# Kernel tuning notes

Measured on AMD Instinct MI355X. Metric: run time of the kernel, lower is better.

Reference implementation:

```python
import jax, jax.numpy as jnp
import numpy as np

D_MODEL = 1024
NUM_HEADS = 16
ROPE_THETA = 10000.0


def setup_inputs() -> dict:
    key = jax.random.key(0)
    ks = jax.random.split(key, 5)
    B, S, D = 4, 2048, D_MODEL
    std = (2.0 / (D * D)) ** 0.5
    return {
        "x": jax.random.normal(ks[0], (B, S, D), dtype=jnp.float32),
        "Wq": jax.random.normal(ks[1], (D, D), dtype=jnp.float32) * std,
        "Wk": jax.random.normal(ks[2], (D, D), dtype=jnp.float32) * std,
        "Wv": jax.random.normal(ks[3], (D, D), dtype=jnp.float32) * std,
        "Wo": jax.random.normal(ks[4], (D, D), dtype=jnp.float32) * std,
    }


def _apply_rope(t, sin, cos):
    # t: [B, H, S, d_k]; sin/cos: [S, d_k//2] (broadcast over B, H)
    e = t[..., 0::2]
    o = t[..., 1::2]
    rot = jnp.stack((e * cos - o * sin, e * sin + o * cos), axis=-1)
    return rot.reshape(t.shape)  # interleave back to d_k


def reference(x, Wq, Wk, Wv, Wo):
    B, S, D = x.shape
    H = NUM_HEADS
    dk = D // H

    def proj(W):
        y = jnp.einsum('bsd,ed->bse', x, W)  # Linear: weight is [out, in]
        return y.reshape(B, S, H, dk).transpose(0, 2, 1, 3)  # [B,H,S,dk]

    q, k, v = proj(Wq), proj(Wk), proj(Wv)

    # RoPE cache (token_positions = arange(S))
    half = dk // 2
    inv_freq = 1.0 / (ROPE_THETA ** (jnp.arange(half, dtype=jnp.float32) * 2.0 / dk))
    angles = jnp.arange(S, dtype=jnp.float32)[:, None] * inv_freq[None, :]  # [S, half]
    sin, cos = jnp.sin(angles), jnp.cos(angles)
    q = _apply_rope(q, sin, cos)
    k = _apply_rope(k, sin, cos)

    # scaled dot-product attention with causal mask
    scores = jnp.einsum('bhqd,bhkd->bhqk', q, k) / jnp.sqrt(jnp.float32(dk))
    causal = jnp.tril(jnp.ones((S, S), dtype=bool))
    scores = jnp.where(causal, scores, jnp.finfo(scores.dtype).min)
    p = jax.nn.softmax(scores, axis=-1)
    out = jnp.einsum('bhqk,bhkd->bhqd', p, v)  # [B,H,S,dk]

    out = out.transpose(0, 2, 1, 3).reshape(B, S, D)
    return jnp.einsum('bsd,ed->bse', out, Wo)
```

## Files before the change

kernel.cpp:

```cpp
#include <hip/hip_runtime.h>

typedef unsigned short u16;
typedef unsigned int   u32;

typedef short    short8 __attribute__((ext_vector_type(8)));
typedef __bf16   bf16x8 __attribute__((ext_vector_type(8)));
typedef _Float16 half8  __attribute__((ext_vector_type(8)));
typedef float    f32x4  __attribute__((ext_vector_type(4)));

#define S_LEN   2048
#define DM      1024
#define NHEAD   16
#define DK      64
#define KDIM    1024

__device__ __forceinline__ u16 f2bf(float f) {
    u32 u = __builtin_bit_cast(u32, f);
    u += 0x7FFFu + ((u >> 16) & 1u);
    return (u16)(u >> 16);
}
__device__ __forceinline__ f32x4 mfma_bf16(short8 a, short8 b, f32x4 c) {
    return __builtin_amdgcn_mfma_f32_16x16x32_bf16(
        __builtin_bit_cast(bf16x8, a), __builtin_bit_cast(bf16x8, b), c, 0, 0, 0);
}
__device__ __forceinline__ f32x4 mfma_f16(half8 a, half8 b, f32x4 c) {
    return __builtin_amdgcn_mfma_f32_16x16x32_f16(a, b, c, 0, 0, 0);
}
__device__ __forceinline__ u32 pk_f16(float a, float b) {
    return __builtin_bit_cast(u32, __builtin_amdgcn_cvt_pkrtz(a, b));
}
__device__ __forceinline__ void gl_lds16(const void* g, void* l) {
    __builtin_amdgcn_global_load_lds(
        (const __attribute__((address_space(1))) u32*)g,
        (__attribute__((address_space(3))) u32*)l, 16, 0, 0);
}
__device__ __forceinline__ void bar_raw() { asm volatile("s_barrier" ::: "memory"); }
__device__ __forceinline__ void wait_vm4() { asm volatile("s_waitcnt vmcnt(4)" ::: "memory"); }
__device__ __forceinline__ void wait_vm0() { asm volatile("s_waitcnt vmcnt(0)" ::: "memory"); }

__device__ __forceinline__ int perm_inv(int rc) {
    const int nt = rc >> 4, mid = (rc >> 2) & 3, r = rc & 3;
    return 32 * (nt >> 1) + 8 * mid + 4 * (nt & 1) + r;
}

__global__ void cvt_all(const float4* __restrict__ x,  const float4* __restrict__ Wq,
                        const float4* __restrict__ Wk, const float4* __restrict__ Wv,
                        const float4* __restrict__ Wo,
                        uint2* __restrict__ oX, uint2* __restrict__ oWcat,
                        uint2* __restrict__ oWo,
                        float* __restrict__ sT, float* __restrict__ cT) {
    const int i = blockIdx.x * 256 + threadIdx.x;
    if (i < 3145728) {
        const float4* in;
        uint2* out;
        if (i < 2097152) {
            in = x + i;  out = oX + i;
        } else {
            const int j = i - 2097152;
            const int w = j >> 18, k = j & 262143;
            in  = (w == 0 ? Wq : w == 1 ? Wk : w == 2 ? Wv : Wo) + k;
            out = (w < 3) ? (oWcat + w * 262144 + k) : (oWo + k);
        }
        float4 f = *in;
        uint2 o;
        o.x = (u32)f2bf(f.x) | ((u32)f2bf(f.y) << 16);
        o.y = (u32)f2bf(f.z) | ((u32)f2bf(f.w) << 16);
        *out = o;
    } else {
        const int idx = i - 3145728;
        const float fi = expf(-(float)(idx >> 11) * 0.287823136624255f);
        const float ang = (float)(idx & 2047) * fi;
        sT[idx] = sinf(ang);
        cT[idx] = cosf(ang);
    }
}

template <int MODE>
__global__ __launch_bounds__(256)
void gemm_nt(const u16* __restrict__ A, const u16* __restrict__ Bw,
             u16* __restrict__ oQ, u16* __restrict__ oK, u16* __restrict__ oVt,
             float* __restrict__ oF,
             const float* __restrict__ ropeS, const float* __restrict__ ropeC) {
    __shared__ u16 As[2][128 * 32];
    __shared__ u16 Bs[2][128 * 32];
    const int tid  = threadIdx.x;
    const int wave = tid >> 6, lane = tid & 63;
    const int quad = lane >> 4, l15 = lane & 15;
    const int wr = wave >> 1, wc = wave & 1;
    const int NX  = (MODE == 0) ? 24 : 8;
    const int lin = (int)blockIdx.x + NX * (int)blockIdx.y;
    const int xcd = lin & 7, idx = lin >> 3;
    const int mbase = (xcd * 8 + idx / NX) * 128;
    const int nbase = (idx % NX) * 128;

    f32x4 acc[4][4];
#pragma unroll
    for (int i = 0; i < 4; i++)
#pragma unroll
        for (int j = 0; j < 4; j++) acc[i][j] = (f32x4)0.0f;

    const int srow0 = wave * 32 + (lane >> 2);
    const int srow1 = srow0 + 16;
    const int scolb = ((lane & 3) ^ ((lane >> 3) & 3)) * 16;
    const int ldsOff = wave * 2048 + lane * 16;
    const u16* gA0 = A  + (size_t)(mbase + srow0) * KDIM;
    const u16* gA1 = A  + (size_t)(mbase + srow1) * KDIM;
    const u16* gB0 = Bw + (size_t)(nbase + srow0) * KDIM;
    const u16* gB1 = Bw + (size_t)(nbase + srow1) * KDIM;
    const int koffq = (quad ^ ((l15 >> 1) & 3)) * 8;

    const int KT = KDIM / 64;
    for (int kt = 0; kt < KT; kt++) {
        const int kk = kt * 64;
        __syncthreads();
#pragma unroll
        for (int s = 0; s < 2; s++) {
            const int ko = kk + s * 32;
            gl_lds16((const char*)(gA0 + ko) + scolb, (char*)As[s] + ldsOff);
            gl_lds16((const char*)(gA1 + ko) + scolb, (char*)As[s] + ldsOff + 1024);
            gl_lds16((const char*)(gB0 + ko) + scolb, (char*)Bs[s] + ldsOff);
            gl_lds16((const char*)(gB1 + ko) + scolb, (char*)Bs[s] + ldsOff + 1024);
        }
        __syncthreads();

        short8 af[4][2], bf[4][2];
#pragma unroll
        for (int s = 0; s < 2; s++) {
#pragma unroll
            for (int mt = 0; mt < 4; mt++)
                af[mt][s] = *(const short8*)&As[s][(wr * 64 + mt * 16 + l15) * 32 + koffq];
#pragma unroll
            for (int nt = 0; nt < 4; nt++)
                bf[nt][s] = *(const short8*)&Bs[s][(wc * 64 + nt * 16 + l15) * 32 + koffq];
        }
#pragma unroll
        for (int s = 0; s < 2; s++)
#pragma unroll
            for (int mt = 0; mt < 4; mt++)
#pragma unroll
                for (int nt = 0; nt < 4; nt++)
                    acc[mt][nt] = mfma_bf16(af[mt][s], bf[nt][s], acc[mt][nt]);
    }

    const int proj_blk = (MODE == 0) ? (nbase >> 10) : 2;

    const float* sB[4];
    const float* cB[4];
    if (MODE == 0 && proj_blk < 2) {
#pragma unroll
        for (int nt = 0; nt < 4; nt++) {
            const int fi = nt * 8 + (l15 >> 1);
            sB[nt] = ropeS + fi * 2048;
            cB[nt] = ropeC + fi * 2048;
        }
    }
    const int par = l15 & 1;

#pragma unroll
    for (int mt = 0; mt < 4; mt++) {
#pragma unroll
        for (int nt = 0; nt < 4; nt++) {
            const int n  = nbase + wc * 64 + nt * 16 + l15;
            const int mb = mbase + wr * 64 + mt * 16 + quad * 4;
            f32x4 v = acc[mt][nt];
            if (MODE == 0) {
                const int e = n & 1023;
                const int h = e >> 6, d = e & 63;
                if (proj_blk == 2) {
                    const int b_ = mb >> 11, s = mb & 2047;
                    const int bh = b_ * NHEAD + h;
                    uint2 pk;
                    pk.x = pk_f16(v[0], v[1]);
                    pk.y = pk_f16(v[2], v[3]);
                    *(uint2*)&oVt[((size_t)bh * DK + d) * S_LEN + s] = pk;
                } else {
                    u16* dst = (proj_blk == 0) ? oQ : oK;
                    float vp[4];
#pragma unroll
                    for (int r = 0; r < 4; r++) vp[r] = __shfl_xor(v[r], 1);
                    const int b_ = mb >> 11, s0 = mb & 2047;
                    const int bh = b_ * NHEAD + h;
                    const f32x4 sn = *(const f32x4*)(sB[nt] + s0);
                    const f32x4 cs = *(const f32x4*)(cB[nt] + s0);
#pragma unroll
                    for (int r = 0; r < 4; r++) {
                        const float res = par ? (vp[r] * sn[r] + v[r] * cs[r])
                                              : (v[r] * cs[r] - vp[r] * sn[r]);
                        dst[((size_t)bh * S_LEN + (s0 + r)) * DK + d] = f2bf(res);
                    }
                }
            } else {
#pragma unroll
                for (int r = 0; r < 4; r++)
                    oF[(size_t)(mb + r) * DM + n] = v[r];
            }
        }
    }
}

__global__ __launch_bounds__(256)
void flash_attn(const u16* __restrict__ Q, const u16* __restrict__ K,
                const u16* __restrict__ Vt, u16* __restrict__ Oc) {
    __shared__ u16 Ks[2][64 * 64];
    __shared__ u16 Vs[2][64 * 64];
    const int lin = (int)blockIdx.x + 64 * (int)blockIdx.y;
    const int xcd = lin & 7, idx = lin >> 3;
    const int bh  = xcd * 8 + (idx & 7);
    const int qt  = 31 - (idx >> 3);
    const int tid  = threadIdx.x;
    const int wave = tid >> 6, lane = tid & 63;
    const int quad = lane >> 4, l15 = lane & 15;
    const int x7 = l15 & 7;
    const size_t headQK = (size_t)bh * S_LEN * DK;
    const size_t headVt = (size_t)bh * DK * S_LEN;
    const int b = bh >> 4, h = bh & 15;
    const float SCL = 0.18033688011112042f;
    const float THRESH = 44.3614195558365f;

    half8 ones;
#pragma unroll
    for (int j = 0; j < 8; j++) ones[j] = (_Float16)1.0f;

    const int rwl  = lane >> 3;
    const int scol = (lane & 7) ^ rwl;
    const int rc0 = wave * 16 + rwl, rc1 = rc0 + 8;
    const u16* gK0 = K  + headQK + (size_t)perm_inv(rc0) * DK + scol * 8;
    const u16* gK1 = K  + headQK + (size_t)perm_inv(rc1) * DK + scol * 8;
    const u16* gV0 = Vt + headVt + (size_t)rc0 * S_LEN + scol * 8;
    const u16* gV1 = Vt + headVt + (size_t)rc1 * S_LEN + scol * 8;
    const int ldsOff = wave * 2048 + lane * 16;
    const int koff0 = (quad ^ x7) * 8;
    const int koff1 = ((4 + quad) ^ x7) * 8;

    short8 qf0, qf1;
    {
        const int qrow = qt * 64 + wave * 16 + l15;
        qf0 = *(const short8*)&Q[headQK + (size_t)qrow * DK + quad * 8];
        qf1 = *(const short8*)&Q[headQK + (size_t)qrow * DK + 32 + quad * 8];
    }

    float m_st = -__builtin_inff();
    f32x4 lacc = (f32x4)0.0f;
    f32x4 oacc[4];
#pragma unroll
    for (int n = 0; n < 4; n++) oacc[n] = (f32x4)0.0f;

    const int NT = qt + 1;
    gl_lds16(gK0, (char*)Ks[0] + ldsOff);
    gl_lds16(gK1, (char*)Ks[0] + ldsOff + 1024);
    gl_lds16(gV0, (char*)Vs[0] + ldsOff);
    gl_lds16(gV1, (char*)Vs[0] + ldsOff + 1024);

    for (int kt = 0; kt < NT; kt++) {
        const int cur = kt & 1, nxt = cur ^ 1;
        bar_raw();
        {
            const int ktn = (kt + 1 < NT) ? kt + 1 : kt;
            gl_lds16(gK0 + (size_t)ktn * 64 * DK, (char*)Ks[nxt] + ldsOff);
            gl_lds16(gK1 + (size_t)ktn * 64 * DK, (char*)Ks[nxt] + ldsOff + 1024);
            gl_lds16(gV0 + ktn * 64,              (char*)Vs[nxt] + ldsOff);
            gl_lds16(gV1 + ktn * 64,              (char*)Vs[nxt] + ldsOff + 1024);
        }
        wait_vm4();
        bar_raw();

        f32x4 sc[4];
        __builtin_amdgcn_s_setprio(1);
#pragma unroll
        for (int nt = 0; nt < 4; nt++) {
            const int rb = (nt * 16 + l15) * 64;
            short8 kf0 = *(const short8*)&Ks[cur][rb + koff0];
            short8 kf1 = *(const short8*)&Ks[cur][rb + koff1];
            f32x4 z = (f32x4)0.0f;
            z = mfma_bf16(kf0, qf0, z);
            z = mfma_bf16(kf1, qf1, z);
            sc[nt] = z;
        }
        __builtin_amdgcn_s_setprio(0);

        if (kt == qt) {
            const int qloc = wave * 16 + l15;
#pragma unroll
            for (int nt = 0; nt < 4; nt++) {
                const int kb = 32 * (nt >> 1) + 8 * quad + 4 * (nt & 1);
#pragma unroll
                for (int r = 0; r < 4; r++)
                    if (kb + r > qloc) sc[nt][r] = -__builtin_inff();
            }
        }
        float mx0 = fmaxf(fmaxf(sc[0][0], sc[0][1]), fmaxf(sc[0][2], sc[0][3]));
        float mx1 = fmaxf(fmaxf(sc[1][0], sc[1][1]), fmaxf(sc[1][2], sc[1][3]));
        float mx2 = fmaxf(fmaxf(sc[2][0], sc[2][1]), fmaxf(sc[2][2], sc[2][3]));
        float mx3 = fmaxf(fmaxf(sc[3][0], sc[3][1]), fmaxf(sc[3][2], sc[3][3]));
        float mx = fmaxf(fmaxf(mx0, mx1), fmaxf(mx2, mx3));
        mx = fmaxf(mx, __shfl_xor(mx, 16));
        mx = fmaxf(mx, __shfl_xor(mx, 32));
        if (!__all(mx - m_st <= THRESH)) {
            const float mn = fmaxf(m_st, mx);
            const float alpha = __builtin_amdgcn_exp2f((m_st - mn) * SCL);
            m_st = mn;
            float alr[4];
#pragma unroll
            for (int r = 0; r < 4; r++) alr[r] = __shfl(alpha, quad * 20 + r);
#pragma unroll
            for (int n = 0; n < 4; n++)
#pragma unroll
                for (int r = 0; r < 4; r++) oacc[n][r] *= alr[r];
#pragma unroll
            for (int r = 0; r < 4; r++) lacc[r] *= alr[r];
        }
        const float msc = m_st * SCL;
#pragma unroll
        for (int nt = 0; nt < 4; nt++)
#pragma unroll
            for (int r = 0; r < 4; r++)
                sc[nt][r] = __builtin_amdgcn_exp2f(
                    __builtin_fmaf(sc[nt][r], SCL, -msc));
        u32 pw[8];
        pw[0] = pk_f16(sc[0][0], sc[0][1]); pw[1] = pk_f16(sc[0][2], sc[0][3]);
        pw[2] = pk_f16(sc[1][0], sc[1][1]); pw[3] = pk_f16(sc[1][2], sc[1][3]);
        pw[4] = pk_f16(sc[2][0], sc[2][1]); pw[5] = pk_f16(sc[2][2], sc[2][3]);
        pw[6] = pk_f16(sc[3][0], sc[3][1]); pw[7] = pk_f16(sc[3][2], sc[3][3]);
        half8 pf0 = __builtin_bit_cast(half8, *(uint4*)&pw[0]);
        half8 pf1 = __builtin_bit_cast(half8, *(uint4*)&pw[4]);

        __builtin_amdgcn_s_setprio(1);
#pragma unroll
        for (int c = 0; c < 2; c++) {
            const half8 pf = c ? pf1 : pf0;
            lacc = mfma_f16(pf, ones, lacc);
            const int voff = ((c * 4 + quad) ^ x7) * 8;
#pragma unroll
            for (int nt2 = 0; nt2 < 4; nt2++) {
                half8 vf = __builtin_bit_cast(half8,
                    *(const short8*)&Vs[cur][(nt2 * 16 + l15) * 64 + voff]);
                oacc[nt2] = mfma_f16(pf, vf, oacc[nt2]);
            }
        }
        __builtin_amdgcn_s_setprio(0);
    }
    wait_vm0();

#pragma unroll
    for (int r = 0; r < 4; r++) {
        const float inv = 1.0f / lacc[r];
        const int s = qt * 64 + wave * 16 + quad * 4 + r;
#pragma unroll
        for (int nt2 = 0; nt2 < 4; nt2++)
            Oc[((size_t)(b * S_LEN + s)) * DM + h * 64 + nt2 * 16 + l15] =
                f2bf(oacc[nt2][r] * inv);
    }
}

#define OFF_XBF   ((size_t)0)
#define OFF_WCAT  ((size_t)8388608)
#define OFF_WO    ((size_t)11534336)
#define OFF_QB    ((size_t)12582912)
#define OFF_KB    ((size_t)20971520)
#define OFF_VT    ((size_t)29360128)
#define OFF_ROPE  ((size_t)37748736)

extern "C" void kernel_launch(void* const* d_in, const int* in_sizes, int n_in,
                              void* d_out, int out_size, void* d_ws, size_t ws_size,
                              hipStream_t stream) {
    const float* x  = (const float*)d_in[0];
    const float* Wq = (const float*)d_in[1];
    const float* Wk = (const float*)d_in[2];
    const float* Wv = (const float*)d_in[3];
    const float* Wo = (const float*)d_in[4];
    u16* ws  = (u16*)d_ws;
    u16* XBF = ws + OFF_XBF;
    u16* WCA = ws + OFF_WCAT;
    u16* WOB = ws + OFF_WO;
    u16* QB  = ws + OFF_QB;
    u16* KB  = ws + OFF_KB;
    u16* VT  = ws + OFF_VT;
    float* ropeS = (float*)(ws + OFF_ROPE);
    float* ropeC = ropeS + 65536;
    u16* AT  = XBF;

    cvt_all<<<12544, 256, 0, stream>>>((const float4*)x, (const float4*)Wq,
                                       (const float4*)Wk, (const float4*)Wv,
                                       (const float4*)Wo,
                                       (uint2*)XBF, (uint2*)WCA, (uint2*)WOB,
                                       ropeS, ropeC);

    gemm_nt<0><<<dim3(24, 64), 256, 0, stream>>>(XBF, WCA, QB, KB, VT, nullptr,
                                                 ropeS, ropeC);
    flash_attn<<<dim3(64, 32), 256, 0, stream>>>(QB, KB, VT, AT);
    gemm_nt<1><<<dim3(8, 64), 256, 0, stream>>>(AT, WOB, nullptr, nullptr, nullptr,
                                                (float*)d_out, nullptr, nullptr);
}
```

Baseline: 257.0 us.

## Share K/V tiles across two query tiles with 512-thread attention blocks

Each flash-attention block now handles 128 query rows with 8 waves instead of 64 rows with 4 waves, so every K/V tile loaded into LDS serves twice as many queries. Each wave now issues half as many global-to-LDS loads per tile, and the wait count is adjusted to match. The lower half of the block skips the final K tile, which lies beyond its causal range. In exchange the grid halves, the causal load is split across blocks more coarsely, and lower-half waves idle at the barriers for that last tile.

```diff
diff --git a/kernel.cpp b/kernel.cpp
--- a/kernel.cpp
+++ b/kernel.cpp
@@ -35,7 +35,7 @@
         (__attribute__((address_space(3))) u32*)l, 16, 0, 0);
 }
 __device__ __forceinline__ void bar_raw() { asm volatile("s_barrier" ::: "memory"); }
-__device__ __forceinline__ void wait_vm4() { asm volatile("s_waitcnt vmcnt(4)" ::: "memory"); }
+__device__ __forceinline__ void wait_vm2() { asm volatile("s_waitcnt vmcnt(2)" ::: "memory"); }
 __device__ __forceinline__ void wait_vm0() { asm volatile("s_waitcnt vmcnt(0)" ::: "memory"); }
 
 __device__ __forceinline__ int perm_inv(int rc) {
@@ -198,7 +198,7 @@
     }
 }
 
-__global__ __launch_bounds__(256)
+__global__ __launch_bounds__(512)
 void flash_attn(const u16* __restrict__ Q, const u16* __restrict__ K,
                 const u16* __restrict__ Vt, u16* __restrict__ Oc) {
     __shared__ u16 Ks[2][64 * 64];
@@ -206,9 +206,10 @@
     const int lin = (int)blockIdx.x + 64 * (int)blockIdx.y;
     const int xcd = lin & 7, idx = lin >> 3;
     const int bh  = xcd * 8 + (idx & 7);
-    const int qt  = 31 - (idx >> 3);
+    const int qt  = 15 - (idx >> 3);
     const int tid  = threadIdx.x;
     const int wave = tid >> 6, lane = tid & 63;
+    const int hh   = wave >> 2, w4 = wave & 3;
     const int quad = lane >> 4, l15 = lane & 15;
     const int x7 = l15 & 7;
     const size_t headQK = (size_t)bh * S_LEN * DK;
@@ -223,18 +224,16 @@
 
     const int rwl  = lane >> 3;
     const int scol = (lane & 7) ^ rwl;
-    const int rc0 = wave * 16 + rwl, rc1 = rc0 + 8;
-    const u16* gK0 = K  + headQK + (size_t)perm_inv(rc0) * DK + scol * 8;
-    const u16* gK1 = K  + headQK + (size_t)perm_inv(rc1) * DK + scol * 8;
-    const u16* gV0 = Vt + headVt + (size_t)rc0 * S_LEN + scol * 8;
-    const u16* gV1 = Vt + headVt + (size_t)rc1 * S_LEN + scol * 8;
-    const int ldsOff = wave * 2048 + lane * 16;
+    const int rc   = wave * 8 + rwl;
+    const u16* gK = K  + headQK + (size_t)perm_inv(rc) * DK + scol * 8;
+    const u16* gV = Vt + headVt + (size_t)rc * S_LEN + scol * 8;
+    const int ldsOff = wave * 1024 + lane * 16;
     const int koff0 = (quad ^ x7) * 8;
     const int koff1 = ((4 + quad) ^ x7) * 8;
 
     short8 qf0, qf1;
     {
-        const int qrow = qt * 64 + wave * 16 + l15;
+        const int qrow = qt * 128 + hh * 64 + w4 * 16 + l15;
         qf0 = *(const short8*)&Q[headQK + (size_t)qrow * DK + quad * 8];
         qf1 = *(const short8*)&Q[headQK + (size_t)qrow * DK + 32 + quad * 8];
     }
@@ -245,24 +244,24 @@
 #pragma unroll
     for (int n = 0; n < 4; n++) oacc[n] = (f32x4)0.0f;
 
-    const int NT = qt + 1;
-    gl_lds16(gK0, (char*)Ks[0] + ldsOff);
-    gl_lds16(gK1, (char*)Ks[0] + ldsOff + 1024);
-    gl_lds16(gV0, (char*)Vs[0] + ldsOff);
-    gl_lds16(gV1, (char*)Vs[0] + ldsOff + 1024);
+    const int NT = 2 * qt + 2;
+    const int skip_kt = (hh == 0) ? (2 * qt + 1) : -1;
+    const int diag_kt = 2 * qt + hh;
+    gl_lds16(gK, (char*)Ks[0] + ldsOff);
+    gl_lds16(gV, (char*)Vs[0] + ldsOff);
 
     for (int kt = 0; kt < NT; kt++) {
         const int cur = kt & 1, nxt = cur ^ 1;
         bar_raw();
         {
             const int ktn = (kt + 1 < NT) ? kt + 1 : kt;
-            gl_lds16(gK0 + (size_t)ktn * 64 * DK, (char*)Ks[nxt] + ldsOff);
-            gl_lds16(gK1 + (size_t)ktn * 64 * DK, (char*)Ks[nxt] + ldsOff + 1024);
-            gl_lds16(gV0 + ktn * 64,              (char*)Vs[nxt] + ldsOff);
-            gl_lds16(gV1 + ktn * 64,              (char*)Vs[nxt] + ldsOff + 1024);
-        }
-        wait_vm4();
+            gl_lds16(gK + (size_t)ktn * 64 * DK, (char*)Ks[nxt] + ldsOff);
+            gl_lds16(gV + ktn * 64,              (char*)Vs[nxt] + ldsOff);
+        }
+        wait_vm2();
         bar_raw();
+
+        if (kt == skip_kt) continue;
 
         f32x4 sc[4];
         __builtin_amdgcn_s_setprio(1);
@@ -278,8 +277,8 @@
         }
         __builtin_amdgcn_s_setprio(0);
 
-        if (kt == qt) {
-            const int qloc = wave * 16 + l15;
+        if (kt == diag_kt) {
+            const int qloc = w4 * 16 + l15;
 #pragma unroll
             for (int nt = 0; nt < 4; nt++) {
                 const int kb = 32 * (nt >> 1) + 8 * quad + 4 * (nt & 1);
@@ -344,7 +343,7 @@
 #pragma unroll
     for (int r = 0; r < 4; r++) {
         const float inv = 1.0f / lacc[r];
-        const int s = qt * 64 + wave * 16 + quad * 4 + r;
+        const int s = qt * 128 + hh * 64 + w4 * 16 + quad * 4 + r;
 #pragma unroll
         for (int nt2 = 0; nt2 < 4; nt2++)
             Oc[((size_t)(b * S_LEN + s)) * DM + h * 64 + nt2 * 16 + l15] =
@@ -387,7 +386,7 @@
 
     gemm_nt<0><<<dim3(24, 64), 256, 0, stream>>>(XBF, WCA, QB, KB, VT, nullptr,
                                                  ropeS, ropeC);
-    flash_attn<<<dim3(64, 32), 256, 0, stream>>>(QB, KB, VT, AT);
+    flash_attn<<<dim3(64, 16), 512, 0, stream>>>(QB, KB, VT, AT);
     gemm_nt<1><<<dim3(8, 64), 256, 0, stream>>>(AT, WOB, nullptr, nullptr, nullptr,
                                                 (float*)d_out, nullptr, nullptr);
 }
```

Result: faster. 245.8 us (median of 3 runs) (-4.3%).
